# Optimization experiments

Hardware: AMD Instinct MI355X
Metric: run time of the kernel (lower is better)

The kernel has to match this reference:

```python
import jax, jax.numpy as jnp
import numpy as np

N2 = 524288   # raw batch (2B)
F = 256       # raw feature dim; concat of halves -> D = 2F
D = 512       # input_dim (gated feature dim)
H_GATE = 64
H_EXP = 128


def _init(key, shape, fan_in):
    return jax.random.normal(key, shape, jnp.float32) / np.sqrt(fan_in)


def setup_inputs() -> dict:
    key = jax.random.key(0)
    ks = jax.random.split(key, 13)
    x = jax.random.normal(ks[0], (N2, F), jnp.float32)
    # gate: Linear(D,64) -> ReLU -> Linear(64,2)
    gw1 = _init(ks[1], (D, H_GATE), D)
    gb1 = jnp.zeros((H_GATE,), jnp.float32)
    gw2 = _init(ks[2], (H_GATE, 2), H_GATE)
    gb2 = jnp.zeros((2,), jnp.float32)
    # expert_a: Linear(D,128) -> ReLU -> Linear(128,2)
    aw1 = _init(ks[3], (D, H_EXP), D)
    ab1 = jnp.zeros((H_EXP,), jnp.float32)
    aw2 = _init(ks[4], (H_EXP, 2), H_EXP)
    ab2 = jnp.zeros((2,), jnp.float32)
    # expert_b: same shapes
    bw1 = _init(ks[5], (D, H_EXP), D)
    bb1 = jnp.zeros((H_EXP,), jnp.float32)
    bw2 = _init(ks[6], (H_EXP, 2), H_EXP)
    bb2 = jnp.zeros((2,), jnp.float32)
    return dict(x=x, gw1=gw1, gb1=gb1, gw2=gw2, gb2=gb2,
                aw1=aw1, ab1=ab1, aw2=aw2, ab2=ab2,
                bw1=bw1, bb1=bb1, bw2=bw2, bb2=bb2)


def reference(x, gw1, gb1, gw2, gb2, aw1, ab1, aw2, ab2, bw1, bb1, bw2, bb2):
    # backbone = identity; concat first and second batch halves along features
    n = x.shape[0]
    xf = jnp.concatenate([x[: n // 2], x[n // 2 :]], axis=1)  # [B, D]
    # hard gate: argmax over 2 logits
    gate_logits = jax.nn.relu(xf @ gw1 + gb1) @ gw2 + gb2  # [B, 2]
    gate_idx = jnp.argmax(gate_logits, axis=1)  # [B]
    # run both tiny experts densely, then mask (same math as masked dispatch)
    out_a = jax.nn.relu(xf @ aw1 + ab1) @ aw2 + ab2  # [B, 2]
    out_b = jax.nn.relu(xf @ bw1 + bb1) @ bw2 + bb2  # [B, 2]
    m_a = (gate_idx == 0)[:, None]
    # rows routed to expert_a fill cols 0:2, rows routed to expert_b fill cols 2:4
    return jnp.concatenate(
        [jnp.where(m_a, out_a, 0.0), jnp.where(m_a, 0.0, out_b)], axis=1
    )  # [B, 4]
```

## Files before the change

### kernel.cpp

```cpp
#include <hip/hip_runtime.h>
#include <hip/hip_bf16.h>

#define HALF_ROWS 262144
#define TAU 0.04f
#define BT_OFF 1024
#define LIST_OFF (BT_OFF + 320 * 512 * 2)

typedef __attribute__((ext_vector_type(8))) short s16x8;
typedef __attribute__((ext_vector_type(4))) float f32x4;

__device__ __forceinline__ unsigned short f2bf(float f) {
  union { float f; unsigned u; } v; v.f = f;
  unsigned r = v.u + 0x7fffu + ((v.u >> 16) & 1u);
  return (unsigned short)(r >> 16);
}

#define GLOAD_LDS16(g, p) \
  __builtin_amdgcn_global_load_lds((const __attribute__((address_space(1))) void*)(g), \
                                   (__attribute__((address_space(3))) void*)(p), 16, 0, 0)

__device__ __forceinline__ s16x8 cvt8(const f32x4& a, const f32x4& b) {
  union { int i[4]; s16x8 v; } u;
  asm("v_cvt_pk_bf16_f32 %0, %1, %2" : "=v"(u.i[0]) : "v"(a[0]), "v"(a[1]));
  asm("v_cvt_pk_bf16_f32 %0, %1, %2" : "=v"(u.i[1]) : "v"(a[2]), "v"(a[3]));
  asm("v_cvt_pk_bf16_f32 %0, %1, %2" : "=v"(u.i[2]) : "v"(b[0]), "v"(b[1]));
  asm("v_cvt_pk_bf16_f32 %0, %1, %2" : "=v"(u.i[3]) : "v"(b[2]), "v"(b[3]));
  return u.v;
}

__global__ void moe_prep(const float* __restrict__ gw1, const float* __restrict__ aw1,
                         const float* __restrict__ bw1, unsigned short* __restrict__ Bf,
                         unsigned* __restrict__ cnt) {
  if (blockIdx.x == 0 && threadIdx.x == 0) *cnt = 0u;
  int idx = blockIdx.x * 512 + threadIdx.x;
  int j = idx & 7, l = (idx >> 3) & 63, ks = (idx >> 9) & 15, cb = idx >> 13;
  int col = cb * 16 + (l & 15);
  int k = ks * 32 + ((l >> 4) << 3) + j;
  float v;
  if (col < 64)       v = gw1[k * 64 + col];
  else if (col < 192) v = aw1[k * 128 + (col - 64)];
  else                v = bw1[k * 128 + (col - 192)];
  Bf[idx] = f2bf(v);
}

__global__ __launch_bounds__(1024, 4) void moe_main(
    const float* __restrict__ x, const unsigned short* __restrict__ Bf,
    const float* __restrict__ gb1, const float* __restrict__ gw2, const float* __restrict__ gb2,
    const float* __restrict__ ab1, const float* __restrict__ aw2, const float* __restrict__ ab2,
    const float* __restrict__ bb1, const float* __restrict__ bw2, const float* __restrict__ bb2,
    float* __restrict__ out, unsigned* __restrict__ cnt, unsigned* __restrict__ list, int cap) {
  __shared__ char Bl[3][20480];

  const int tid = threadIdx.x;
  const int w = tid >> 6, l = tid & 63;
  const int lo = l & 15, hi = l >> 4;
  const long row0 = (long)blockIdx.x * 256 + w * 16 + lo;
  const float* ap = x + row0 * 256 + hi * 8;

  const unsigned short* bsrc = Bf + l * 8;
  auto issueB = [&](int kc) {
    char* dst = Bl[kc % 3];
    GLOAD_LDS16(bsrc + ((size_t)(w * 16 + kc) << 9), dst + w * 1024);
    if (w < 4)
      GLOAD_LDS16(bsrc + ((size_t)((16 + w) * 16 + kc) << 9), dst + (16 + w) * 1024);
  };

  f32x4 cur0, cur1, nxt0, nxt1;
  auto loadA = [&](int kc, f32x4& d0, f32x4& d1) {
    const float* p = ap + (kc & 7) * 32 + (kc >= 8 ? (long)HALF_ROWS * 256 : 0L);
    d0 = *(const f32x4*)p;
    d1 = *(const f32x4*)(p + 4);
  };

  f32x4 acc[20];
#pragma unroll
  for (int ct = 0; ct < 20; ++ct) acc[ct] = (f32x4){0.f, 0.f, 0.f, 0.f};

  loadA(0, cur0, cur1);
  issueB(0);
  issueB(1);
  if (w < 4) asm volatile("s_waitcnt vmcnt(2)" ::: "memory");
  else       asm volatile("s_waitcnt vmcnt(1)" ::: "memory");
  __builtin_amdgcn_s_barrier();

#pragma unroll 1
  for (int kc = 0; kc < 16; ++kc) {
    if (kc + 2 < 16) issueB(kc + 2);
    if (kc + 1 < 16) loadA(kc + 1, nxt0, nxt1);
    asm volatile("" ::: "memory");
    s16x8 af = cvt8(cur0, cur1);
    const char* buf = Bl[kc % 3];
#pragma unroll
    for (int ct = 0; ct < 20; ++ct) {
      s16x8 bf = *(const s16x8*)(buf + (ct << 10) + (l << 4));
      acc[ct] = __builtin_amdgcn_mfma_f32_16x16x32_bf16(af, bf, acc[ct], 0, 0, 0);
    }
    cur0 = nxt0; cur1 = nxt1;
    if (kc < 15) __builtin_amdgcn_s_barrier();
  }

  float pg0[4] = {0,0,0,0}, pg1[4] = {0,0,0,0};
  float pa0[4] = {0,0,0,0}, pa1[4] = {0,0,0,0};
  float pq0[4] = {0,0,0,0}, pq1[4] = {0,0,0,0};
#pragma unroll
  for (int ct = 0; ct < 20; ++ct) {
    int col = ct * 16 + lo;
    float b1, w0, w1;
    if (ct < 4)       { b1 = gb1[col];        w0 = gw2[col * 2];        w1 = gw2[col * 2 + 1]; }
    else if (ct < 12) { int c = col - 64;  b1 = ab1[c]; w0 = aw2[c * 2]; w1 = aw2[c * 2 + 1]; }
    else              { int c = col - 192; b1 = bb1[c]; w0 = bw2[c * 2]; w1 = bw2[c * 2 + 1]; }
#pragma unroll
    for (int j = 0; j < 4; ++j) {
      float h = fmaxf(acc[ct][j] + b1, 0.f);
      float t0 = h * w0, t1 = h * w1;
      if (ct < 4)       { pg0[j] += t0; pg1[j] += t1; }
      else if (ct < 12) { pa0[j] += t0; pa1[j] += t1; }
      else              { pq0[j] += t0; pq1[j] += t1; }
    }
  }
#pragma unroll
  for (int m = 1; m < 16; m <<= 1)
#pragma unroll
    for (int j = 0; j < 4; ++j) {
      pg0[j] += __shfl_xor(pg0[j], m); pg1[j] += __shfl_xor(pg1[j], m);
      pa0[j] += __shfl_xor(pa0[j], m); pa1[j] += __shfl_xor(pa1[j], m);
      pq0[j] += __shfl_xor(pq0[j], m); pq1[j] += __shfl_xor(pq1[j], m);
    }
  if (lo == 0) {
    float g2a = gb2[0], g2b = gb2[1];
    float a2a = ab2[0], a2b = ab2[1];
    float b2a = bb2[0], b2b = bb2[1];
#pragma unroll
    for (int j = 0; j < 4; ++j) {
      long grow = ((long)blockIdx.x * 256 + w * 16) + hi * 4 + j;
      float gl0 = pg0[j] + g2a, gl1 = pg1[j] + g2b;
      float fa0 = pa0[j] + a2a, fa1 = pa1[j] + a2b;
      float fb0 = pq0[j] + b2a, fb1 = pq1[j] + b2b;
      bool m0 = gl0 >= gl1;
      f32x4 o;
      o[0] = m0 ? fa0 : 0.f; o[1] = m0 ? fa1 : 0.f;
      o[2] = m0 ? 0.f : fb0; o[3] = m0 ? 0.f : fb1;
      *(f32x4*)(out + grow * 4) = o;
      float diff = gl0 - gl1;
      if (fabsf(diff) < TAU && cap > 0) {
        unsigned u = atomicAdd(cnt, 1u);
        if (u < (unsigned)cap) {
          unsigned* e = list + (size_t)u * 8;
          e[0] = (unsigned)grow;
          float* ef = (float*)(e + 4);
          ef[0] = fa0; ef[1] = fa1; ef[2] = fb0; ef[3] = fb1;
        }
      }
    }
  }
}

__global__ void moe_fixup(const float* __restrict__ x,
                          const float* __restrict__ gw1, const float* __restrict__ gb1,
                          const float* __restrict__ gw2, const float* __restrict__ gb2,
                          float* __restrict__ out, const unsigned* __restrict__ cnt,
                          const unsigned* __restrict__ list, int cap) {
  unsigned n = *cnt;
  if (n > (unsigned)cap) n = (unsigned)cap;
  const int l = threadIdx.x & 63;
  const int wid = blockIdx.x * (blockDim.x >> 6) + (threadIdx.x >> 6);
  const int nw = gridDim.x * (blockDim.x >> 6);
  for (unsigned e = wid; e < n; e += nw) {
    const unsigned* ent = list + (size_t)e * 8;
    unsigned row = ent[0];
    const float* ef = (const float*)(ent + 4);
    const float* xr0 = x + (long)row * 256;
    const float* xr1 = x + ((long)row + HALF_ROWS) * 256;
    double a[8] = {0, 0, 0, 0, 0, 0, 0, 0};
#pragma unroll 2
    for (int d = 0; d < 256; d += 8)
#pragma unroll
      for (int q = 0; q < 8; ++q)
        a[q] += (double)xr0[d + q] * (double)gw1[(d + q) * 64 + l];
#pragma unroll 2
    for (int d = 0; d < 256; d += 8)
#pragma unroll
      for (int q = 0; q < 8; ++q)
        a[q] += (double)xr1[d + q] * (double)gw1[(d + 256 + q) * 64 + l];
    double h = ((a[0] + a[1]) + (a[2] + a[3])) + ((a[4] + a[5]) + (a[6] + a[7]))
             + (double)gb1[l];
    h = h > 0.0 ? h : 0.0;
    double t0 = h * (double)gw2[l * 2];
    double t1 = h * (double)gw2[l * 2 + 1];
#pragma unroll
    for (int m = 1; m < 64; m <<= 1) {
      t0 += __shfl_xor(t0, m);
      t1 += __shfl_xor(t1, m);
    }
    if (l == 0) {
      bool m0 = (t0 + (double)gb2[0]) >= (t1 + (double)gb2[1]);
      f32x4 o;
      o[0] = m0 ? ef[0] : 0.f; o[1] = m0 ? ef[1] : 0.f;
      o[2] = m0 ? 0.f : ef[2]; o[3] = m0 ? 0.f : ef[3];
      *(f32x4*)(out + (size_t)row * 4) = o;
    }
  }
}

extern "C" void kernel_launch(void* const* d_in, const int* in_sizes, int n_in,
                              void* d_out, int out_size, void* d_ws, size_t ws_size,
                              hipStream_t stream) {
  const float* x   = (const float*)d_in[0];
  const float* gw1 = (const float*)d_in[1];
  const float* gb1 = (const float*)d_in[2];
  const float* gw2 = (const float*)d_in[3];
  const float* gb2 = (const float*)d_in[4];
  const float* aw1 = (const float*)d_in[5];
  const float* ab1 = (const float*)d_in[6];
  const float* aw2 = (const float*)d_in[7];
  const float* ab2 = (const float*)d_in[8];
  const float* bw1 = (const float*)d_in[9];
  const float* bb1 = (const float*)d_in[10];
  const float* bw2 = (const float*)d_in[11];
  const float* bb2 = (const float*)d_in[12];
  float* out = (float*)d_out;

  unsigned char* ws = (unsigned char*)d_ws;
  unsigned* cnt = (unsigned*)ws;
  unsigned short* Bf = (unsigned short*)(ws + BT_OFF);
  unsigned* list = (unsigned*)(ws + LIST_OFF);
  long cap_l = ((long)ws_size - (long)LIST_OFF) / 32;
  int cap = cap_l < 0 ? 0 : (cap_l > 262144 ? 262144 : (int)cap_l);

  moe_prep<<<320, 512, 0, stream>>>(gw1, aw1, bw1, Bf, cnt);
  moe_main<<<1024, 1024, 0, stream>>>(x, Bf, gb1, gw2, gb2, ab1, aw2, ab2,
                                      bb1, bw2, bb2, out, cnt, list, cap);
  moe_fixup<<<2048, 256, 0, stream>>>(x, gw1, gb1, gw2, gb2, out, cnt, list, cap);
}
```

Measured before the change: 329.5 us.

## Pre-convert x to bf16 in MFMA fragment layout and deepen LDS pipeline

Adds a separate kernel that converts x from fp32 to bf16 and writes it in a per-wave fragment-ordered layout in workspace. The main GEMM kernel then loads A fragments with one contiguous 16-byte load instead of converting inline. It also moves to a 4-stage LDS ring for B with explicit vmcnt waits and sched barriers, and spreads the B loads over 10 waves. This removes the conversion and strided fp32 loads from the main loop, at the cost of an extra full pass that writes and re-reads a 256MB intermediate, plus a much larger workspace requirement.

```diff
diff --git a/kernel.cpp b/kernel.cpp
--- a/kernel.cpp
+++ b/kernel.cpp
@@ -4,7 +4,8 @@
 #define HALF_ROWS 262144
 #define TAU 0.04f
 #define BT_OFF 1024
-#define LIST_OFF (BT_OFF + 320 * 512 * 2)
+#define XBF_OFF (1 << 20)
+#define LIST_OFF (XBF_OFF + 268435456)
 
 typedef __attribute__((ext_vector_type(8))) short s16x8;
 typedef __attribute__((ext_vector_type(4))) float f32x4;
@@ -43,61 +44,97 @@
   Bf[idx] = f2bf(v);
 }
 
+__global__ __launch_bounds__(256) void moe_convert(const float* __restrict__ x,
+                                                   unsigned short* __restrict__ xbff) {
+  const long stride = 4096L * 256;
+  const long t = (long)blockIdx.x * 256 + threadIdx.x;
+#pragma unroll 1
+  for (int b = 0; b < 2; ++b) {
+    f32x4 v[8][2];
+    const long c0 = t + (long)b * 8 * stride;
+#pragma unroll
+    for (int u = 0; u < 8; ++u) {
+      const f32x4* p = (const f32x4*)(x + (c0 + u * stride) * 8);
+      v[u][0] = __builtin_nontemporal_load(p);
+      v[u][1] = __builtin_nontemporal_load(p + 1);
+    }
+#pragma unroll
+    for (int u = 0; u < 8; ++u) {
+      long cc = c0 + u * stride;
+      long srow = cc >> 5;
+      int k8 = (int)(cc & 31) << 3;
+      long drow; int koff;
+      if (srow >= HALF_ROWS) { drow = srow - HALF_ROWS; koff = 256 + k8; }
+      else                   { drow = srow;             koff = k8; }
+      long G = drow >> 4;
+      int kc = koff >> 5, slot = (koff >> 3) & 3;
+      int ln = (int)(drow & 15) + slot * 16;
+      *(s16x8*)(xbff + (G << 13) + (kc << 9) + (ln << 3)) = cvt8(v[u][0], v[u][1]);
+    }
+  }
+}
+
+#define WAITLOHI(VLO, VHI)                                              \
+  if (w < 10) asm volatile("s_waitcnt vmcnt(" #VLO ")" ::: "memory");   \
+  else        asm volatile("s_waitcnt vmcnt(" #VHI ")" ::: "memory");
+
+#define STEP(KC, CUR, NXT, DO_LOADA, DO_ISSUEB, VLO, VHI)                          \
+  {                                                                                \
+    if (DO_LOADA)                                                                  \
+      asm volatile("global_load_dwordx4 %0, %1, off"                               \
+                   : "=&v"(NXT) : "v"(ap + (((KC) + 1) << 9)));                    \
+    if (DO_ISSUEB) issueB((KC) + 2);                                               \
+    WAITLOHI(VLO, VHI)                                                             \
+    __builtin_amdgcn_sched_barrier(0);                                             \
+    __builtin_amdgcn_s_barrier();                                                  \
+    __builtin_amdgcn_sched_barrier(0);                                             \
+    const char* buf = Bl[(KC) & 3];                                                \
+    _Pragma("unroll")                                                              \
+    for (int ct = 0; ct < 20; ++ct) {                                              \
+      s16x8 bfv = *(const s16x8*)(buf + (ct << 10) + (l << 4));                    \
+      acc[ct] = __builtin_amdgcn_mfma_f32_16x16x32_bf16(CUR, bfv, acc[ct], 0, 0, 0);\
+    }                                                                              \
+  }
+
 __global__ __launch_bounds__(1024, 4) void moe_main(
-    const float* __restrict__ x, const unsigned short* __restrict__ Bf,
+    const unsigned short* __restrict__ xbff, const unsigned short* __restrict__ Bf,
     const float* __restrict__ gb1, const float* __restrict__ gw2, const float* __restrict__ gb2,
     const float* __restrict__ ab1, const float* __restrict__ aw2, const float* __restrict__ ab2,
     const float* __restrict__ bb1, const float* __restrict__ bw2, const float* __restrict__ bb2,
     float* __restrict__ out, unsigned* __restrict__ cnt, unsigned* __restrict__ list, int cap) {
-  __shared__ char Bl[3][20480];
+  __shared__ char Bl[4][20480];
 
   const int tid = threadIdx.x;
   const int w = tid >> 6, l = tid & 63;
   const int lo = l & 15, hi = l >> 4;
-  const long row0 = (long)blockIdx.x * 256 + w * 16 + lo;
-  const float* ap = x + row0 * 256 + hi * 8;
+  const unsigned short* ap = xbff + ((size_t)(blockIdx.x * 16 + w) << 13) + (l << 3);
 
   const unsigned short* bsrc = Bf + l * 8;
   auto issueB = [&](int kc) {
-    char* dst = Bl[kc % 3];
-    GLOAD_LDS16(bsrc + ((size_t)(w * 16 + kc) << 9), dst + w * 1024);
-    if (w < 4)
-      GLOAD_LDS16(bsrc + ((size_t)((16 + w) * 16 + kc) << 9), dst + (16 + w) * 1024);
+    if (w < 10) {
+      char* dst = Bl[kc & 3] + w * 2048;
+      const unsigned short* g = bsrc + ((size_t)((2 * w) * 16 + kc) << 9);
+      GLOAD_LDS16(g, dst);
+      GLOAD_LDS16(g + 8192, dst + 1024);
+    }
   };
 
-  f32x4 cur0, cur1, nxt0, nxt1;
-  auto loadA = [&](int kc, f32x4& d0, f32x4& d1) {
-    const float* p = ap + (kc & 7) * 32 + (kc >= 8 ? (long)HALF_ROWS * 256 : 0L);
-    d0 = *(const f32x4*)p;
-    d1 = *(const f32x4*)(p + 4);
-  };
-
   f32x4 acc[20];
 #pragma unroll
   for (int ct = 0; ct < 20; ++ct) acc[ct] = (f32x4){0.f, 0.f, 0.f, 0.f};
 
-  loadA(0, cur0, cur1);
+  s16x8 a0, a1;
+  asm volatile("global_load_dwordx4 %0, %1, off" : "=&v"(a0) : "v"(ap));
   issueB(0);
   issueB(1);
-  if (w < 4) asm volatile("s_waitcnt vmcnt(2)" ::: "memory");
-  else       asm volatile("s_waitcnt vmcnt(1)" ::: "memory");
-  __builtin_amdgcn_s_barrier();
 
 #pragma unroll 1
-  for (int kc = 0; kc < 16; ++kc) {
-    if (kc + 2 < 16) issueB(kc + 2);
-    if (kc + 1 < 16) loadA(kc + 1, nxt0, nxt1);
-    asm volatile("" ::: "memory");
-    s16x8 af = cvt8(cur0, cur1);
-    const char* buf = Bl[kc % 3];
-#pragma unroll
-    for (int ct = 0; ct < 20; ++ct) {
-      s16x8 bf = *(const s16x8*)(buf + (ct << 10) + (l << 4));
-      acc[ct] = __builtin_amdgcn_mfma_f32_16x16x32_bf16(af, bf, acc[ct], 0, 0, 0);
-    }
-    cur0 = nxt0; cur1 = nxt1;
-    if (kc < 15) __builtin_amdgcn_s_barrier();
-  }
+  for (int kc = 0; kc < 14; kc += 2) {
+    STEP(kc,     a0, a1, true, true, 5, 1)
+    STEP(kc + 1, a1, a0, true, true, 5, 1)
+  }
+  STEP(14, a0, a1, true,  false, 3, 1)
+  STEP(15, a1, a0, false, false, 0, 0)
 
   float pg0[4] = {0,0,0,0}, pg1[4] = {0,0,0,0};
   float pa0[4] = {0,0,0,0}, pa1[4] = {0,0,0,0};
@@ -223,12 +260,14 @@
   unsigned char* ws = (unsigned char*)d_ws;
   unsigned* cnt = (unsigned*)ws;
   unsigned short* Bf = (unsigned short*)(ws + BT_OFF);
+  unsigned short* xbff = (unsigned short*)(ws + XBF_OFF);
   unsigned* list = (unsigned*)(ws + LIST_OFF);
   long cap_l = ((long)ws_size - (long)LIST_OFF) / 32;
   int cap = cap_l < 0 ? 0 : (cap_l > 262144 ? 262144 : (int)cap_l);
 
   moe_prep<<<320, 512, 0, stream>>>(gw1, aw1, bw1, Bf, cnt);
-  moe_main<<<1024, 1024, 0, stream>>>(x, Bf, gb1, gw2, gb2, ab1, aw2, ab2,
+  moe_convert<<<4096, 256, 0, stream>>>(x, xbff);
+  moe_main<<<1024, 1024, 0, stream>>>(xbff, Bf, gb1, gw2, gb2, ab1, aw2, ab2,
                                       bb1, bw2, bb2, out, cnt, list, cap);
   moe_fixup<<<2048, 256, 0, stream>>>(x, gw1, gb1, gw2, gb2, out, cnt, list, cap);
 }
```

Result: slower. 464.5 us (+41.0%).

## Process two row tiles per wave with 4-stage B buffer and inline-asm A loads

Applied to the files above, without the earlier changes.

Each wave now computes two 16-row tiles (32 rows), so every LDS B fragment read feeds two MFMAs, halving LDS traffic per MFMA. The block shrinks to 512 threads (8 waves), B staging moves to a 4-deep ring spread across all waves, and A loads are issued as inline-asm dwordx4 with explicit vmcnt waits and a barrier placed before compute. This raises register pressure (40 accumulators) and lowers wave count per block, trading occupancy for reuse and deeper prefetch.

```diff
diff --git a/kernel.cpp b/kernel.cpp
--- a/kernel.cpp
+++ b/kernel.cpp
@@ -43,116 +43,143 @@
   Bf[idx] = f2bf(v);
 }
 
-__global__ __launch_bounds__(1024, 4) void moe_main(
+#define WAITB(V3, V2)                                                  \
+  if (w < 4) asm volatile("s_waitcnt vmcnt(" #V3 ")" ::: "memory");    \
+  else       asm volatile("s_waitcnt vmcnt(" #V2 ")" ::: "memory");
+
+#define STEP(KC, C0A, C0B, C1A, C1B, N0A, N0B, N1A, N1B, DO_A, DO_B, V3, V2)       \
+  {                                                                                \
+    if (DO_A) {                                                                    \
+      const int kn = (KC) + 1;                                                     \
+      const float* pb = (kn < 8) ? apA : apA2;                                     \
+      const float* p0 = pb + (kn & 7) * 32;                                        \
+      const float* p1 = p0 + 16 * 256;                                             \
+      asm volatile("global_load_dwordx4 %0, %1, off" : "=&v"(N0A) : "v"(p0));      \
+      asm volatile("global_load_dwordx4 %0, %1, off" : "=&v"(N0B) : "v"(p0 + 4));  \
+      asm volatile("global_load_dwordx4 %0, %1, off" : "=&v"(N1A) : "v"(p1));      \
+      asm volatile("global_load_dwordx4 %0, %1, off" : "=&v"(N1B) : "v"(p1 + 4));  \
+    }                                                                              \
+    if (DO_B) issueB((KC) + 2);                                                    \
+    WAITB(V3, V2)                                                                  \
+    __builtin_amdgcn_sched_barrier(0);                                             \
+    __builtin_amdgcn_s_barrier();                                                  \
+    __builtin_amdgcn_sched_barrier(0);                                             \
+    s16x8 af0 = cvt8(C0A, C0B);                                                    \
+    s16x8 af1 = cvt8(C1A, C1B);                                                    \
+    const char* buf = Bl[(KC) & 3];                                                \
+    _Pragma("unroll")                                                              \
+    for (int ct = 0; ct < 20; ++ct) {                                              \
+      s16x8 bfv = *(const s16x8*)(buf + (ct << 10) + (l << 4));                    \
+      acc0[ct] = __builtin_amdgcn_mfma_f32_16x16x32_bf16(af0, bfv, acc0[ct], 0, 0, 0); \
+      acc1[ct] = __builtin_amdgcn_mfma_f32_16x16x32_bf16(af1, bfv, acc1[ct], 0, 0, 0); \
+    }                                                                              \
+  }
+
+__global__ __launch_bounds__(512, 2) void moe_main(
     const float* __restrict__ x, const unsigned short* __restrict__ Bf,
     const float* __restrict__ gb1, const float* __restrict__ gw2, const float* __restrict__ gb2,
     const float* __restrict__ ab1, const float* __restrict__ aw2, const float* __restrict__ ab2,
     const float* __restrict__ bb1, const float* __restrict__ bw2, const float* __restrict__ bb2,
     float* __restrict__ out, unsigned* __restrict__ cnt, unsigned* __restrict__ list, int cap) {
-  __shared__ char Bl[3][20480];
+  __shared__ char Bl[4][20480];
 
   const int tid = threadIdx.x;
   const int w = tid >> 6, l = tid & 63;
   const int lo = l & 15, hi = l >> 4;
-  const long row0 = (long)blockIdx.x * 256 + w * 16 + lo;
-  const float* ap = x + row0 * 256 + hi * 8;
+  const long r0 = (long)blockIdx.x * 256 + w * 32;
+  const float* apA  = x + (r0 + lo) * 256 + hi * 8;
+  const float* apA2 = apA + (long)HALF_ROWS * 256;
 
   const unsigned short* bsrc = Bf + l * 8;
+  const int s0 = (w < 4) ? w * 3 : 12 + (w - 4) * 2;
+  const int ns = (w < 4) ? 3 : 2;
   auto issueB = [&](int kc) {
-    char* dst = Bl[kc % 3];
-    GLOAD_LDS16(bsrc + ((size_t)(w * 16 + kc) << 9), dst + w * 1024);
-    if (w < 4)
-      GLOAD_LDS16(bsrc + ((size_t)((16 + w) * 16 + kc) << 9), dst + (16 + w) * 1024);
+    char* dst = Bl[kc & 3] + s0 * 1024;
+    const unsigned short* g = bsrc + ((size_t)(s0 * 16 + kc) << 9);
+#pragma unroll
+    for (int s = 0; s < 3; ++s)
+      if (s < ns) GLOAD_LDS16(g + ((size_t)s << 13), dst + s * 1024);
   };
 
-  f32x4 cur0, cur1, nxt0, nxt1;
-  auto loadA = [&](int kc, f32x4& d0, f32x4& d1) {
-    const float* p = ap + (kc & 7) * 32 + (kc >= 8 ? (long)HALF_ROWS * 256 : 0L);
-    d0 = *(const f32x4*)p;
-    d1 = *(const f32x4*)(p + 4);
-  };
-
-  f32x4 acc[20];
-#pragma unroll
-  for (int ct = 0; ct < 20; ++ct) acc[ct] = (f32x4){0.f, 0.f, 0.f, 0.f};
-
-  loadA(0, cur0, cur1);
+  f32x4 acc0[20], acc1[20];
+#pragma unroll
+  for (int ct = 0; ct < 20; ++ct) {
+    acc0[ct] = (f32x4){0.f, 0.f, 0.f, 0.f};
+    acc1[ct] = (f32x4){0.f, 0.f, 0.f, 0.f};
+  }
+
+  f32x4 xA0, xA1, xA2, xA3, xB0, xB1, xB2, xB3;
+  asm volatile("global_load_dwordx4 %0, %1, off" : "=&v"(xA0) : "v"(apA));
+  asm volatile("global_load_dwordx4 %0, %1, off" : "=&v"(xA1) : "v"(apA + 4));
+  asm volatile("global_load_dwordx4 %0, %1, off" : "=&v"(xA2) : "v"(apA + 16 * 256));
+  asm volatile("global_load_dwordx4 %0, %1, off" : "=&v"(xA3) : "v"(apA + 16 * 256 + 4));
   issueB(0);
   issueB(1);
-  if (w < 4) asm volatile("s_waitcnt vmcnt(2)" ::: "memory");
-  else       asm volatile("s_waitcnt vmcnt(1)" ::: "memory");
-  __builtin_amdgcn_s_barrier();
 
 #pragma unroll 1
-  for (int kc = 0; kc < 16; ++kc) {
-    if (kc + 2 < 16) issueB(kc + 2);
-    if (kc + 1 < 16) loadA(kc + 1, nxt0, nxt1);
-    asm volatile("" ::: "memory");
-    s16x8 af = cvt8(cur0, cur1);
-    const char* buf = Bl[kc % 3];
-#pragma unroll
-    for (int ct = 0; ct < 20; ++ct) {
-      s16x8 bf = *(const s16x8*)(buf + (ct << 10) + (l << 4));
-      acc[ct] = __builtin_amdgcn_mfma_f32_16x16x32_bf16(af, bf, acc[ct], 0, 0, 0);
-    }
-    cur0 = nxt0; cur1 = nxt1;
-    if (kc < 15) __builtin_amdgcn_s_barrier();
-  }
-
-  float pg0[4] = {0,0,0,0}, pg1[4] = {0,0,0,0};
-  float pa0[4] = {0,0,0,0}, pa1[4] = {0,0,0,0};
-  float pq0[4] = {0,0,0,0}, pq1[4] = {0,0,0,0};
-#pragma unroll
-  for (int ct = 0; ct < 20; ++ct) {
-    int col = ct * 16 + lo;
-    float b1, w0, w1;
-    if (ct < 4)       { b1 = gb1[col];        w0 = gw2[col * 2];        w1 = gw2[col * 2 + 1]; }
-    else if (ct < 12) { int c = col - 64;  b1 = ab1[c]; w0 = aw2[c * 2]; w1 = aw2[c * 2 + 1]; }
-    else              { int c = col - 192; b1 = bb1[c]; w0 = bw2[c * 2]; w1 = bw2[c * 2 + 1]; }
-#pragma unroll
-    for (int j = 0; j < 4; ++j) {
-      float h = fmaxf(acc[ct][j] + b1, 0.f);
-      float t0 = h * w0, t1 = h * w1;
-      if (ct < 4)       { pg0[j] += t0; pg1[j] += t1; }
-      else if (ct < 12) { pa0[j] += t0; pa1[j] += t1; }
-      else              { pq0[j] += t0; pq1[j] += t1; }
-    }
-  }
-#pragma unroll
-  for (int m = 1; m < 16; m <<= 1)
-#pragma unroll
-    for (int j = 0; j < 4; ++j) {
-      pg0[j] += __shfl_xor(pg0[j], m); pg1[j] += __shfl_xor(pg1[j], m);
-      pa0[j] += __shfl_xor(pa0[j], m); pa1[j] += __shfl_xor(pa1[j], m);
-      pq0[j] += __shfl_xor(pq0[j], m); pq1[j] += __shfl_xor(pq1[j], m);
-    }
-  if (lo == 0) {
-    float g2a = gb2[0], g2b = gb2[1];
-    float a2a = ab2[0], a2b = ab2[1];
-    float b2a = bb2[0], b2b = bb2[1];
-#pragma unroll
-    for (int j = 0; j < 4; ++j) {
-      long grow = ((long)blockIdx.x * 256 + w * 16) + hi * 4 + j;
-      float gl0 = pg0[j] + g2a, gl1 = pg1[j] + g2b;
-      float fa0 = pa0[j] + a2a, fa1 = pa1[j] + a2b;
-      float fb0 = pq0[j] + b2a, fb1 = pq1[j] + b2b;
-      bool m0 = gl0 >= gl1;
-      f32x4 o;
-      o[0] = m0 ? fa0 : 0.f; o[1] = m0 ? fa1 : 0.f;
-      o[2] = m0 ? 0.f : fb0; o[3] = m0 ? 0.f : fb1;
-      *(f32x4*)(out + grow * 4) = o;
-      float diff = gl0 - gl1;
-      if (fabsf(diff) < TAU && cap > 0) {
-        unsigned u = atomicAdd(cnt, 1u);
-        if (u < (unsigned)cap) {
-          unsigned* e = list + (size_t)u * 8;
-          e[0] = (unsigned)grow;
-          float* ef = (float*)(e + 4);
-          ef[0] = fa0; ef[1] = fa1; ef[2] = fb0; ef[3] = fb1;
-        }
-      }
-    }
-  }
+  for (int kc = 0; kc < 14; kc += 2) {
+    STEP(kc,     xA0, xA1, xA2, xA3, xB0, xB1, xB2, xB3, true, true, 10, 8)
+    STEP(kc + 1, xB0, xB1, xB2, xB3, xA0, xA1, xA2, xA3, true, true, 10, 8)
+  }
+  STEP(14, xA0, xA1, xA2, xA3, xB0, xB1, xB2, xB3, true,  false, 7, 6)
+  STEP(15, xB0, xB1, xB2, xB3, xA0, xA1, xA2, xA3, false, false, 0, 0)
+
+  float b1v, w0v, w1v;
+#define EPI(ACC, RT)                                                              \
+  {                                                                               \
+    float pg0[4] = {0,0,0,0}, pg1[4] = {0,0,0,0};                                 \
+    float pa0[4] = {0,0,0,0}, pa1[4] = {0,0,0,0};                                 \
+    float pq0[4] = {0,0,0,0}, pq1[4] = {0,0,0,0};                                 \
+    _Pragma("unroll")                                                             \
+    for (int ct = 0; ct < 20; ++ct) {                                             \
+      int col = ct * 16 + lo;                                                     \
+      if (ct < 4)       { b1v = gb1[col];        w0v = gw2[col * 2];        w1v = gw2[col * 2 + 1]; } \
+      else if (ct < 12) { int c = col - 64;  b1v = ab1[c]; w0v = aw2[c * 2]; w1v = aw2[c * 2 + 1]; } \
+      else              { int c = col - 192; b1v = bb1[c]; w0v = bw2[c * 2]; w1v = bw2[c * 2 + 1]; } \
+      _Pragma("unroll")                                                           \
+      for (int j = 0; j < 4; ++j) {                                               \
+        float h = fmaxf(ACC[ct][j] + b1v, 0.f);                                   \
+        float t0 = h * w0v, t1 = h * w1v;                                         \
+        if (ct < 4)       { pg0[j] += t0; pg1[j] += t1; }                         \
+        else if (ct < 12) { pa0[j] += t0; pa1[j] += t1; }                         \
+        else              { pq0[j] += t0; pq1[j] += t1; }                         \
+      }                                                                           \
+    }                                                                             \
+    _Pragma("unroll")                                                             \
+    for (int m = 1; m < 16; m <<= 1)                                              \
+      _Pragma("unroll")                                                           \
+      for (int j = 0; j < 4; ++j) {                                               \
+        pg0[j] += __shfl_xor(pg0[j], m); pg1[j] += __shfl_xor(pg1[j], m);         \
+        pa0[j] += __shfl_xor(pa0[j], m); pa1[j] += __shfl_xor(pa1[j], m);         \
+        pq0[j] += __shfl_xor(pq0[j], m); pq1[j] += __shfl_xor(pq1[j], m);         \
+      }                                                                           \
+    if (lo == 0) {                                                                \
+      _Pragma("unroll")                                                           \
+      for (int j = 0; j < 4; ++j) {                                               \
+        long grow = r0 + (RT) * 16 + hi * 4 + j;                                  \
+        float gl0 = pg0[j] + gb2[0], gl1 = pg1[j] + gb2[1];                       \
+        float fa0 = pa0[j] + ab2[0], fa1 = pa1[j] + ab2[1];                       \
+        float fb0 = pq0[j] + bb2[0], fb1 = pq1[j] + bb2[1];                       \
+        bool m0 = gl0 >= gl1;                                                     \
+        f32x4 o;                                                                  \
+        o[0] = m0 ? fa0 : 0.f; o[1] = m0 ? fa1 : 0.f;                             \
+        o[2] = m0 ? 0.f : fb0; o[3] = m0 ? 0.f : fb1;                             \
+        *(f32x4*)(out + grow * 4) = o;                                            \
+        float diff = gl0 - gl1;                                                   \
+        if (fabsf(diff) < TAU && cap > 0) {                                       \
+          unsigned u = atomicAdd(cnt, 1u);                                        \
+          if (u < (unsigned)cap) {                                                \
+            unsigned* e = list + (size_t)u * 8;                                   \
+            e[0] = (unsigned)grow;                                                \
+            float* ef = (float*)(e + 4);                                          \
+            ef[0] = fa0; ef[1] = fa1; ef[2] = fb0; ef[3] = fb1;                   \
+          }                                                                       \
+        }                                                                         \
+      }                                                                           \
+    }                                                                             \
+  }
+  EPI(acc0, 0)
+  EPI(acc1, 1)
 }
 
 __global__ void moe_fixup(const float* __restrict__ x,
@@ -228,7 +255,7 @@
   int cap = cap_l < 0 ? 0 : (cap_l > 262144 ? 262144 : (int)cap_l);
 
   moe_prep<<<320, 512, 0, stream>>>(gw1, aw1, bw1, Bf, cnt);
-  moe_main<<<1024, 1024, 0, stream>>>(x, Bf, gb1, gw2, gb2, ab1, aw2, ab2,
-                                      bb1, bw2, bb2, out, cnt, list, cap);
+  moe_main<<<1024, 512, 0, stream>>>(x, Bf, gb1, gw2, gb2, ab1, aw2, ab2,
+                                     bb1, bw2, bb2, out, cnt, list, cap);
   moe_fixup<<<2048, 256, 0, stream>>>(x, gw1, gb1, gw2, gb2, out, cnt, list, cap);
 }
```

Result: faster. 294.3 us (-10.7%).

## Warp-specialize main kernel into producer loaders and MFMA consumer waves

Applied to the files above, without the earlier changes.

Splits each 768-thread block into 4 producer waves that load x rows, convert them to bf16 into double-buffered LDS, and stream weight tiles into triple-buffered LDS. The other 8 consumer waves only read LDS fragments and issue MFMAs. Blocks now cover 128 rows, so the grid doubles. The aim is to keep the matrix units fed while the loads are in flight, hiding global latency. The cost is extra LDS traffic for the A operand, a barrier on every k-chunk, and fewer waves doing compute.

```diff
diff --git a/kernel.cpp b/kernel.cpp
--- a/kernel.cpp
+++ b/kernel.cpp
@@ -5,6 +5,7 @@
 #define TAU 0.04f
 #define BT_OFF 1024
 #define LIST_OFF (BT_OFF + 320 * 512 * 2)
+#define NC 16
 
 typedef __attribute__((ext_vector_type(8))) short s16x8;
 typedef __attribute__((ext_vector_type(4))) float f32x4;
@@ -43,112 +44,147 @@
   Bf[idx] = f2bf(v);
 }
 
-__global__ __launch_bounds__(1024, 4) void moe_main(
+__global__ __launch_bounds__(768, 3) void moe_main(
     const float* __restrict__ x, const unsigned short* __restrict__ Bf,
     const float* __restrict__ gb1, const float* __restrict__ gw2, const float* __restrict__ gb2,
     const float* __restrict__ ab1, const float* __restrict__ aw2, const float* __restrict__ ab2,
     const float* __restrict__ bb1, const float* __restrict__ bw2, const float* __restrict__ bb2,
     float* __restrict__ out, unsigned* __restrict__ cnt, unsigned* __restrict__ list, int cap) {
-  __shared__ char Bl[3][20480];
+  __shared__ char Asl[2][8192];
+  __shared__ char Bsl[3][20480];
 
   const int tid = threadIdx.x;
   const int w = tid >> 6, l = tid & 63;
   const int lo = l & 15, hi = l >> 4;
-  const long row0 = (long)blockIdx.x * 256 + w * 16 + lo;
-  const float* ap = x + row0 * 256 + hi * 8;
-
-  const unsigned short* bsrc = Bf + l * 8;
-  auto issueB = [&](int kc) {
-    char* dst = Bl[kc % 3];
-    GLOAD_LDS16(bsrc + ((size_t)(w * 16 + kc) << 9), dst + w * 1024);
-    if (w < 4)
-      GLOAD_LDS16(bsrc + ((size_t)((16 + w) * 16 + kc) << 9), dst + (16 + w) * 1024);
-  };
-
-  f32x4 cur0, cur1, nxt0, nxt1;
-  auto loadA = [&](int kc, f32x4& d0, f32x4& d1) {
-    const float* p = ap + (kc & 7) * 32 + (kc >= 8 ? (long)HALF_ROWS * 256 : 0L);
-    d0 = *(const f32x4*)p;
-    d1 = *(const f32x4*)(p + 4);
-  };
-
-  f32x4 acc[20];
-#pragma unroll
-  for (int ct = 0; ct < 20; ++ct) acc[ct] = (f32x4){0.f, 0.f, 0.f, 0.f};
-
-  loadA(0, cur0, cur1);
-  issueB(0);
-  issueB(1);
-  if (w < 4) asm volatile("s_waitcnt vmcnt(2)" ::: "memory");
-  else       asm volatile("s_waitcnt vmcnt(1)" ::: "memory");
-  __builtin_amdgcn_s_barrier();
+  const long br = (long)blockIdx.x * 128;
+
+  if (w < 4) {
+    const float* apg0 = x + (br + w * 32 + lo) * 256 + hi * 8;
+    const unsigned short* bsrc = Bf + l * 8;
+    const int cb0 = w * 5;
+
+    f32x4 sA[4], sB[4];
+#define ISSUE_A(KC, S)                                                             \
+    {                                                                              \
+      const float* pb = ((KC) < 8) ? apg0 : (apg0 + (long)HALF_ROWS * 256);        \
+      const float* p0 = pb + ((KC) & 7) * 32;                                      \
+      const float* p1 = p0 + 16 * 256;                                             \
+      asm volatile("global_load_dwordx4 %0, %1, off" : "=&v"(S[0]) : "v"(p0));     \
+      asm volatile("global_load_dwordx4 %0, %1, off" : "=&v"(S[1]) : "v"(p0 + 4)); \
+      asm volatile("global_load_dwordx4 %0, %1, off" : "=&v"(S[2]) : "v"(p1));     \
+      asm volatile("global_load_dwordx4 %0, %1, off" : "=&v"(S[3]) : "v"(p1 + 4)); \
+    }
+    auto issueB = [&](int kc) {
+      char* dst = Bsl[((unsigned)kc) % 3u] + cb0 * 1024;
+#pragma unroll
+      for (int s = 0; s < 5; ++s)
+        GLOAD_LDS16(bsrc + (((size_t)((cb0 + s) * 16 + kc)) << 9), dst + s * 1024);
+    };
+#define COMMIT_A(KC, S)                                                            \
+    {                                                                              \
+      char* dst = Asl[(KC) & 1];                                                   \
+      s16x8 v0 = cvt8(S[0], S[1]);                                                 \
+      s16x8 v1 = cvt8(S[2], S[3]);                                                 \
+      *(s16x8*)(dst + (w * 2) * 1024 + l * 16) = v0;                               \
+      *(s16x8*)(dst + (w * 2 + 1) * 1024 + l * 16) = v1;                           \
+    }
+#define PWAIT(N) asm volatile("s_waitcnt vmcnt(" #N ")" ::: "memory"); \
+                 __builtin_amdgcn_sched_barrier(0)
+#define PBAR()   asm volatile("s_waitcnt lgkmcnt(0)" ::: "memory");    \
+                 __builtin_amdgcn_s_barrier()
+
+    ISSUE_A(0, sA) issueB(0);
+    ISSUE_A(1, sB) issueB(1);
+    PWAIT(9);
+    COMMIT_A(0, sA)
+    PBAR();
 
 #pragma unroll 1
-  for (int kc = 0; kc < 16; ++kc) {
-    if (kc + 2 < 16) issueB(kc + 2);
-    if (kc + 1 < 16) loadA(kc + 1, nxt0, nxt1);
-    asm volatile("" ::: "memory");
-    s16x8 af = cvt8(cur0, cur1);
-    const char* buf = Bl[kc % 3];
+    for (int kc = 0; kc < 14; kc += 2) {
+      ISSUE_A(kc + 2, sA) issueB(kc + 2);
+      PWAIT(9);
+      COMMIT_A(kc + 1, sB)
+      PBAR();
+      if (kc + 3 < NC) {
+        ISSUE_A(kc + 3, sB) issueB(kc + 3);
+        PWAIT(9);
+      } else {
+        PWAIT(0);
+      }
+      COMMIT_A(kc + 2, sA)
+      PBAR();
+    }
+    PWAIT(0);
+    COMMIT_A(15, sB)
+    PBAR();
+  } else {
+    const int cw = w - 4;
+    f32x4 acc[20];
+#pragma unroll
+    for (int ct = 0; ct < 20; ++ct) acc[ct] = (f32x4){0.f, 0.f, 0.f, 0.f};
+
+#pragma unroll 1
+    for (int kc = 0; kc < NC; ++kc) {
+      __builtin_amdgcn_s_barrier();
+      asm volatile("" ::: "memory");
+      const char* ab = Asl[kc & 1];
+      const char* bb = Bsl[((unsigned)kc) % 3u];
+      s16x8 af = *(const s16x8*)(ab + cw * 1024 + l * 16);
+#pragma unroll
+      for (int ct = 0; ct < 20; ++ct) {
+        s16x8 bf = *(const s16x8*)(bb + ct * 1024 + l * 16);
+        acc[ct] = __builtin_amdgcn_mfma_f32_16x16x32_bf16(af, bf, acc[ct], 0, 0, 0);
+      }
+    }
+
+    float pg0[4] = {0,0,0,0}, pg1[4] = {0,0,0,0};
+    float pa0[4] = {0,0,0,0}, pa1[4] = {0,0,0,0};
+    float pq0[4] = {0,0,0,0}, pq1[4] = {0,0,0,0};
 #pragma unroll
     for (int ct = 0; ct < 20; ++ct) {
-      s16x8 bf = *(const s16x8*)(buf + (ct << 10) + (l << 4));
-      acc[ct] = __builtin_amdgcn_mfma_f32_16x16x32_bf16(af, bf, acc[ct], 0, 0, 0);
-    }
-    cur0 = nxt0; cur1 = nxt1;
-    if (kc < 15) __builtin_amdgcn_s_barrier();
-  }
-
-  float pg0[4] = {0,0,0,0}, pg1[4] = {0,0,0,0};
-  float pa0[4] = {0,0,0,0}, pa1[4] = {0,0,0,0};
-  float pq0[4] = {0,0,0,0}, pq1[4] = {0,0,0,0};
-#pragma unroll
-  for (int ct = 0; ct < 20; ++ct) {
-    int col = ct * 16 + lo;
-    float b1, w0, w1;
-    if (ct < 4)       { b1 = gb1[col];        w0 = gw2[col * 2];        w1 = gw2[col * 2 + 1]; }
-    else if (ct < 12) { int c = col - 64;  b1 = ab1[c]; w0 = aw2[c * 2]; w1 = aw2[c * 2 + 1]; }
-    else              { int c = col - 192; b1 = bb1[c]; w0 = bw2[c * 2]; w1 = bw2[c * 2 + 1]; }
-#pragma unroll
-    for (int j = 0; j < 4; ++j) {
-      float h = fmaxf(acc[ct][j] + b1, 0.f);
-      float t0 = h * w0, t1 = h * w1;
-      if (ct < 4)       { pg0[j] += t0; pg1[j] += t1; }
-      else if (ct < 12) { pa0[j] += t0; pa1[j] += t1; }
-      else              { pq0[j] += t0; pq1[j] += t1; }
-    }
-  }
-#pragma unroll
-  for (int m = 1; m < 16; m <<= 1)
-#pragma unroll
-    for (int j = 0; j < 4; ++j) {
-      pg0[j] += __shfl_xor(pg0[j], m); pg1[j] += __shfl_xor(pg1[j], m);
-      pa0[j] += __shfl_xor(pa0[j], m); pa1[j] += __shfl_xor(pa1[j], m);
-      pq0[j] += __shfl_xor(pq0[j], m); pq1[j] += __shfl_xor(pq1[j], m);
-    }
-  if (lo == 0) {
-    float g2a = gb2[0], g2b = gb2[1];
-    float a2a = ab2[0], a2b = ab2[1];
-    float b2a = bb2[0], b2b = bb2[1];
-#pragma unroll
-    for (int j = 0; j < 4; ++j) {
-      long grow = ((long)blockIdx.x * 256 + w * 16) + hi * 4 + j;
-      float gl0 = pg0[j] + g2a, gl1 = pg1[j] + g2b;
-      float fa0 = pa0[j] + a2a, fa1 = pa1[j] + a2b;
-      float fb0 = pq0[j] + b2a, fb1 = pq1[j] + b2b;
-      bool m0 = gl0 >= gl1;
-      f32x4 o;
-      o[0] = m0 ? fa0 : 0.f; o[1] = m0 ? fa1 : 0.f;
-      o[2] = m0 ? 0.f : fb0; o[3] = m0 ? 0.f : fb1;
-      *(f32x4*)(out + grow * 4) = o;
-      float diff = gl0 - gl1;
-      if (fabsf(diff) < TAU && cap > 0) {
-        unsigned u = atomicAdd(cnt, 1u);
-        if (u < (unsigned)cap) {
-          unsigned* e = list + (size_t)u * 8;
-          e[0] = (unsigned)grow;
-          float* ef = (float*)(e + 4);
-          ef[0] = fa0; ef[1] = fa1; ef[2] = fb0; ef[3] = fb1;
+      int col = ct * 16 + lo;
+      float b1, w0, w1;
+      if (ct < 4)       { b1 = gb1[col];        w0 = gw2[col * 2];        w1 = gw2[col * 2 + 1]; }
+      else if (ct < 12) { int c = col - 64;  b1 = ab1[c]; w0 = aw2[c * 2]; w1 = aw2[c * 2 + 1]; }
+      else              { int c = col - 192; b1 = bb1[c]; w0 = bw2[c * 2]; w1 = bw2[c * 2 + 1]; }
+#pragma unroll
+      for (int j = 0; j < 4; ++j) {
+        float h = fmaxf(acc[ct][j] + b1, 0.f);
+        float t0 = h * w0, t1 = h * w1;
+        if (ct < 4)       { pg0[j] += t0; pg1[j] += t1; }
+        else if (ct < 12) { pa0[j] += t0; pa1[j] += t1; }
+        else              { pq0[j] += t0; pq1[j] += t1; }
+      }
+    }
+#pragma unroll
+    for (int m = 1; m < 16; m <<= 1)
+#pragma unroll
+      for (int j = 0; j < 4; ++j) {
+        pg0[j] += __shfl_xor(pg0[j], m); pg1[j] += __shfl_xor(pg1[j], m);
+        pa0[j] += __shfl_xor(pa0[j], m); pa1[j] += __shfl_xor(pa1[j], m);
+        pq0[j] += __shfl_xor(pq0[j], m); pq1[j] += __shfl_xor(pq1[j], m);
+      }
+    if (lo == 0) {
+#pragma unroll
+      for (int j = 0; j < 4; ++j) {
+        long grow = br + cw * 16 + hi * 4 + j;
+        float gl0 = pg0[j] + gb2[0], gl1 = pg1[j] + gb2[1];
+        float fa0 = pa0[j] + ab2[0], fa1 = pa1[j] + ab2[1];
+        float fb0 = pq0[j] + bb2[0], fb1 = pq1[j] + bb2[1];
+        bool m0 = gl0 >= gl1;
+        f32x4 o;
+        o[0] = m0 ? fa0 : 0.f; o[1] = m0 ? fa1 : 0.f;
+        o[2] = m0 ? 0.f : fb0; o[3] = m0 ? 0.f : fb1;
+        *(f32x4*)(out + grow * 4) = o;
+        float diff = gl0 - gl1;
+        if (fabsf(diff) < TAU && cap > 0) {
+          unsigned u = atomicAdd(cnt, 1u);
+          if (u < (unsigned)cap) {
+            unsigned* e = list + (size_t)u * 8;
+            e[0] = (unsigned)grow;
+            float* ef = (float*)(e + 4);
+            ef[0] = fa0; ef[1] = fa1; ef[2] = fb0; ef[3] = fb1;
+          }
         }
       }
     }
@@ -228,7 +264,7 @@
   int cap = cap_l < 0 ? 0 : (cap_l > 262144 ? 262144 : (int)cap_l);
 
   moe_prep<<<320, 512, 0, stream>>>(gw1, aw1, bw1, Bf, cnt);
-  moe_main<<<1024, 1024, 0, stream>>>(x, Bf, gb1, gw2, gb2, ab1, aw2, ab2,
-                                      bb1, bw2, bb2, out, cnt, list, cap);
+  moe_main<<<2048, 768, 0, stream>>>(x, Bf, gb1, gw2, gb2, ab1, aw2, ab2,
+                                     bb1, bw2, bb2, out, cnt, list, cap);
   moe_fixup<<<2048, 256, 0, stream>>>(x, gw1, gb1, gw2, gb2, out, cnt, list, cap);
 }
```

Result: faster. 285.2 us (-13.4%).
